# Kernel optimization log

Measured on AMD Instinct MI355X. Metric: run time of the kernel, lower is better.

## Reference

```python
import jax, jax.numpy as jnp
import numpy as np

N_LAYERS = 6
D_T = 6144   # d_transcoder (features per layer)
D_M = 768    # d_model (residual stream)
TOK = 128    # tokens (batch*seq)


def setup_inputs() -> dict:
    key = jax.random.key(0)
    k_x, k_enc, k_dec = jax.random.split(key, 3)
    x = jax.random.normal(k_x, (N_LAYERS, TOK, D_M), jnp.float32)
    W_enc = jax.random.normal(k_enc, (N_LAYERS, D_T, D_M), jnp.float32) * 0.02
    b_enc = jnp.zeros((N_LAYERS, D_T), jnp.float32)
    b_dec = jnp.zeros((N_LAYERS, D_M), jnp.float32)
    # Padded cross-layer decoder: W_dec[i, j] is the decoder from features at
    # layer i writing into layer j's MLP output; only j >= i is valid
    # (original stores a ragged list of [d_transcoder, n_layers - i, d_model]).
    W_dec = jax.random.normal(k_dec, (N_LAYERS, N_LAYERS, D_T, D_M), jnp.float32) * 0.02
    dec_mask = jnp.triu(jnp.ones((N_LAYERS, N_LAYERS), dtype=bool))  # mask[i, j] = (j >= i)
    W_dec = jnp.where(dec_mask[:, :, None, None], W_dec, 0.0)
    return {"x": x, "W_enc": W_enc, "b_enc": b_enc, "b_dec": b_dec,
            "W_dec": W_dec, "dec_mask": dec_mask}


def reference(x, W_enc, b_enc, b_dec, W_dec, dec_mask):
    # Encode: per-layer feature activations [n_layers, tok, d_transcoder]
    acts = jax.nn.relu(jnp.einsum('lnd,lfd->lnf', x, W_enc) + b_enc[:, None, :])
    # Decode: layer-i features write to all layers j >= i (mask enforces triangle)
    Wd = jnp.where(dec_mask[:, :, None, None], W_dec, 0.0)
    recon = jnp.einsum('inf,ijfd->jnd', acts, Wd) + b_dec[:, None, :]
    return recon  # [n_layers, tok, d_model]
```

## Files before the change

### kernel.cpp

```cpp
#include <hip/hip_runtime.h>
#include <hip/hip_bf16.h>

#define NL 6
#define DT 6144
#define DM 768
#define TOK 128

#define EF 32
#define EK 256
#define ENST (DM / EK)
#define NVE (2 * ENST)

#define TD 256
#define NTD 3
#define FC 768
#define NFC 8
#define NSTEP (FC / 32)
#define TILE_ELEMS (TOK * TD)

using bf16x8 = __attribute__((ext_vector_type(8))) short;
using f32x4  = __attribute__((ext_vector_type(4))) float;

typedef unsigned int u32;
typedef __attribute__((address_space(1))) const u32 gu32;
typedef __attribute__((address_space(3))) u32 lu32;

__device__ __forceinline__ void stage16(const float* g, float* l) {
  __builtin_amdgcn_global_load_lds((gu32*)g, (lu32*)l, 16, 0, 0);
}

#define ISSUE_FENCE() asm volatile("" ::: "memory")
#define VWAIT8() asm volatile("s_waitcnt vmcnt(8)" ::: "memory")
#define VWAIT0() asm volatile("s_waitcnt vmcnt(0)" ::: "memory")
#define RBAR()   asm volatile("s_barrier" ::: "memory")

__device__ __forceinline__ short f2bf(float f) {
  union { float f; unsigned u; } c; c.f = f;
  unsigned u = c.u;
  u += 0x7fffu + ((u >> 16) & 1u);
  return (short)(u >> 16);
}

__device__ __forceinline__ float bf2f(ushort u) {
  union { unsigned u; float f; } c; c.u = ((unsigned)u) << 16;
  return c.f;
}

__global__ void initcvt_k(const float* __restrict__ b_dec,
                          const float* __restrict__ x,
                          float* __restrict__ out, ushort* __restrict__ xb) {
  int idx = blockIdx.x * 256 + threadIdx.x;
  if (idx < NL * TOK * DM) {
    out[idx] = b_dec[(idx / (TOK * DM)) * DM + (idx % DM)];
    xb[idx] = (ushort)f2bf(x[idx]);
  }
}

__global__ __launch_bounds__(256, 2) void encode_k(
    const ushort* __restrict__ xb, const float* __restrict__ W_enc,
    const float* __restrict__ b_enc, ushort* __restrict__ acts)
{
  __shared__ float lw[2][EF][EK];

  const int l  = blockIdx.x / 96;
  const int fp = (blockIdx.x % 96) * 64;
  const int w    = threadIdx.x >> 6;
  const int lane = threadIdx.x & 63;
  const int lo = lane & 15, hi = lane >> 4;

  const float*  We = W_enc + ((size_t)l * DT + fp) * DM;
  const ushort* Xb = xb + (size_t)l * TOK * DM;

  f32x4 acc[2][2];
  #pragma unroll
  for (int mi = 0; mi < 2; ++mi)
    #pragma unroll
    for (int ni = 0; ni < 2; ++ni)
      acc[mi][ni] = f32x4{0.f, 0.f, 0.f, 0.f};

  #pragma unroll
  for (int q = 0; q < 8; ++q) {
    const int row = w * 8 + q;
    stage16(We + (size_t)row * DM + (lane ^ (row & 7)) * 4, &lw[0][row][0]);
  }
  __syncthreads();

  int cur = 0;
  #pragma unroll 1
  for (int v = 0; v < NVE; ++v) {
    const int tt = v / ENST;
    const int st = v % ENST;

    if (v + 1 < NVE) {
      const int tt2 = (v + 1) / ENST;
      const int st2 = (v + 1) % ENST;
      #pragma unroll
      for (int q = 0; q < 8; ++q) {
        const int row = w * 8 + q;
        stage16(We + (size_t)(tt2 * EF + row) * DM + st2 * EK + (lane ^ (row & 7)) * 4,
                &lw[cur ^ 1][row][0]);
      }
    }

    const int sw = lo & 7;
    #pragma unroll
    for (int ks = 0; ks < EK / 32; ++ks) {
      bf16x8 a[2], b[2];
      #pragma unroll
      for (int mi = 0; mi < 2; ++mi)
        a[mi] = *(const bf16x8*)(Xb + (size_t)(w * 32 + mi * 16 + lo) * DM
                                 + st * EK + ks * 32 + hi * 8);
      #pragma unroll
      for (int ni = 0; ni < 2; ++ni) {
        const int c0 = (ks * 8 + hi * 2) ^ sw;
        const int c1 = (ks * 8 + hi * 2 + 1) ^ sw;
        const float4 b0 = *(const float4*)&lw[cur][ni * 16 + lo][c0 * 4];
        const float4 b1 = *(const float4*)&lw[cur][ni * 16 + lo][c1 * 4];
        b[ni][0] = f2bf(b0.x); b[ni][1] = f2bf(b0.y);
        b[ni][2] = f2bf(b0.z); b[ni][3] = f2bf(b0.w);
        b[ni][4] = f2bf(b1.x); b[ni][5] = f2bf(b1.y);
        b[ni][6] = f2bf(b1.z); b[ni][7] = f2bf(b1.w);
      }

      #pragma unroll
      for (int mi = 0; mi < 2; ++mi)
        #pragma unroll
        for (int ni = 0; ni < 2; ++ni)
          acc[mi][ni] = __builtin_amdgcn_mfma_f32_16x16x32_bf16(a[mi], b[ni], acc[mi][ni], 0, 0, 0);
    }

    if (st == ENST - 1) {
      #pragma unroll
      for (int ni = 0; ni < 2; ++ni) {
        const int f = fp + tt * EF + ni * 16 + lo;
        const float bias = b_enc[l * DT + f];
        #pragma unroll
        for (int mi = 0; mi < 2; ++mi) {
          #pragma unroll
          for (int rr = 0; rr < 4; ++rr) {
            const int n = w * 32 + mi * 16 + hi * 4 + rr;
            float vv = acc[mi][ni][rr] + bias;
            vv = vv > 0.f ? vv : 0.f;
            acts[((size_t)l * TOK + n) * DT + f] = (ushort)f2bf(vv);
            acc[mi][ni][rr] = 0.f;
          }
        }
      }
    }

    __syncthreads();
    cur ^= 1;
  }
}

__device__ const int PI_[21]  = {0,0,0,0,0,0, 1,1,1,1,1, 2,2,2,2, 3,3,3, 4,4, 5};
__device__ const int PJ_[21]  = {0,1,2,3,4,5, 1,2,3,4,5, 2,3,4,5, 3,4,5, 4,5, 5};
__device__ const int OFFI_[6] = {0, 6, 11, 15, 18, 20};

__global__ __launch_bounds__(256, 2) void decode_part_k(
    const ushort* __restrict__ acts, const float* __restrict__ W_dec,
    ushort* __restrict__ part)
{
  __shared__ float lw[2][32][TD];

  const int xcd = blockIdx.x & 7;
  const int idx = blockIdx.x >> 3;
  const int logical = xcd * 63 + idx;
  const int p  = logical / (NFC * NTD);
  const int rm = logical % (NFC * NTD);
  const int c  = rm / NTD;
  const int t  = rm % NTD;
  const int i = PI_[p], j = PJ_[p];
  const int w = threadIdx.x >> 6;
  const int lane = threadIdx.x & 63;
  const int lo = lane & 15, hi = lane >> 4;
  const int fb = c * FC;
  (void)j;

  const float*  Wb = W_dec + ((size_t)(i * NL + j) * DT + fb) * DM + t * TD;
  const ushort* Ab = acts + (size_t)i * TOK * DT + fb;

  f32x4 acc[8][4];
  #pragma unroll
  for (int mi = 0; mi < 8; ++mi)
    #pragma unroll
    for (int ni = 0; ni < 4; ++ni)
      acc[mi][ni] = f32x4{0.f, 0.f, 0.f, 0.f};

  #pragma unroll
  for (int q = 0; q < 8; ++q) {
    const int row = w * 8 + q;
    stage16(Wb + (size_t)row * DM + lane * 4, &lw[0][row][0]);
  }

  int cur = 0;
  #pragma unroll 1
  for (int s = 0; s < NSTEP; ++s) {
    bf16x8 a[8];
    #pragma unroll
    for (int mi = 0; mi < 8; ++mi)
      a[mi] = *(const bf16x8*)(Ab + (size_t)(mi * 16 + lo) * DT + s * 32 + hi * 8);
    ISSUE_FENCE();

    if (s + 1 < NSTEP) {
      const float* Ws = Wb + (size_t)(s + 1) * 32 * DM;
      #pragma unroll
      for (int q = 0; q < 8; ++q) {
        const int row = w * 8 + q;
        stage16(Ws + (size_t)row * DM + lane * 4, &lw[cur ^ 1][row][0]);
      }
      VWAIT8();
    } else {
      VWAIT0();
    }
    RBAR();

    bf16x8 bb[4];
    #pragma unroll
    for (int ni = 0; ni < 4; ++ni) {
      const int col = w * 64 + ni * 16 + lo;
      #pragma unroll
      for (int e = 0; e < 8; ++e)
        bb[ni][e] = f2bf(lw[cur][hi * 8 + e][col]);
    }

    #pragma unroll
    for (int mi = 0; mi < 8; ++mi)
      #pragma unroll
      for (int ni = 0; ni < 4; ++ni)
        acc[mi][ni] = __builtin_amdgcn_mfma_f32_16x16x32_bf16(a[mi], bb[ni], acc[mi][ni], 0, 0, 0);

    RBAR();
    cur ^= 1;
  }

  ushort* pp = part + (size_t)logical * TILE_ELEMS;
  #pragma unroll
  for (int ni = 0; ni < 4; ++ni) {
    const int dl = w * 64 + ni * 16 + lo;
    #pragma unroll
    for (int mi = 0; mi < 8; ++mi)
      #pragma unroll
      for (int rr = 0; rr < 4; ++rr)
        pp[(size_t)(mi * 16 + hi * 4 + rr) * TD + dl] = (ushort)f2bf(acc[mi][ni][rr]);
  }
}

__global__ void reduce_k(const ushort* __restrict__ part,
                         const float* __restrict__ b_dec,
                         float* __restrict__ out)
{
  const int idx = blockIdx.x * 256 + threadIdx.x;
  if (idx >= NL * TOK * DM) return;
  const int j   = idx / (TOK * DM);
  const int rem = idx % (TOK * DM);
  const int n   = rem / DM;
  const int d   = rem % DM;
  const int t   = d >> 8;
  const int dl  = d & (TD - 1);

  float s = b_dec[j * DM + d];
  for (int i = 0; i <= j; ++i) {
    const int p = OFFI_[i] + (j - i);
    const ushort* pb = part + ((size_t)(p * NFC) * NTD + t) * TILE_ELEMS
                       + (size_t)n * TD + dl;
    #pragma unroll
    for (int c = 0; c < NFC; ++c)
      s += bf2f(pb[(size_t)c * NTD * TILE_ELEMS]);
  }
  out[idx] = s;
}

__global__ __launch_bounds__(256, 2) void decode_atomic_k(
    const ushort* __restrict__ acts, const float* __restrict__ W_dec,
    float* __restrict__ out)
{
  __shared__ float lw[2][32][TD];

  const int bid = blockIdx.x;
  const int p  = bid / (NTD * NFC);
  const int rm = bid % (NTD * NFC);
  const int c  = rm / NTD;
  const int t  = rm % NTD;
  const int i = PI_[p], j = PJ_[p];
  const int w = threadIdx.x >> 6;
  const int lane = threadIdx.x & 63;
  const int lo = lane & 15, hi = lane >> 4;
  const int fb = c * FC;

  const float*  Wb = W_dec + ((size_t)(i * NL + j) * DT + fb) * DM + t * TD;
  const ushort* Ab = acts + (size_t)i * TOK * DT + fb;

  f32x4 acc[8][4];
  #pragma unroll
  for (int mi = 0; mi < 8; ++mi)
    #pragma unroll
    for (int ni = 0; ni < 4; ++ni)
      acc[mi][ni] = f32x4{0.f, 0.f, 0.f, 0.f};

  #pragma unroll
  for (int q = 0; q < 8; ++q) {
    const int row = w * 8 + q;
    stage16(Wb + (size_t)row * DM + lane * 4, &lw[0][row][0]);
  }
  __syncthreads();

  int cur = 0;
  #pragma unroll 1
  for (int s = 0; s < NSTEP; ++s) {
    if (s + 1 < NSTEP) {
      const float* Ws = Wb + (size_t)(s + 1) * 32 * DM;
      #pragma unroll
      for (int q = 0; q < 8; ++q) {
        const int row = w * 8 + q;
        stage16(Ws + (size_t)row * DM + lane * 4, &lw[cur ^ 1][row][0]);
      }
    }

    bf16x8 a[8];
    #pragma unroll
    for (int mi = 0; mi < 8; ++mi)
      a[mi] = *(const bf16x8*)(Ab + (size_t)(mi * 16 + lo) * DT + s * 32 + hi * 8);

    bf16x8 bb[4];
    #pragma unroll
    for (int ni = 0; ni < 4; ++ni) {
      const int col = w * 64 + ni * 16 + lo;
      #pragma unroll
      for (int e = 0; e < 8; ++e)
        bb[ni][e] = f2bf(lw[cur][hi * 8 + e][col]);
    }

    #pragma unroll
    for (int mi = 0; mi < 8; ++mi)
      #pragma unroll
      for (int ni = 0; ni < 4; ++ni)
        acc[mi][ni] = __builtin_amdgcn_mfma_f32_16x16x32_bf16(a[mi], bb[ni], acc[mi][ni], 0, 0, 0);

    __syncthreads();
    cur ^= 1;
  }

  float* oj = out + (size_t)j * TOK * DM;
  #pragma unroll
  for (int ni = 0; ni < 4; ++ni) {
    const int d = t * TD + w * 64 + ni * 16 + lo;
    #pragma unroll
    for (int mi = 0; mi < 8; ++mi)
      #pragma unroll
      for (int rr = 0; rr < 4; ++rr)
        atomicAdd(oj + (size_t)(mi * 16 + hi * 4 + rr) * DM + d, acc[mi][ni][rr]);
  }
}

extern "C" void kernel_launch(void* const* d_in, const int* in_sizes, int n_in,
                              void* d_out, int out_size, void* d_ws, size_t ws_size,
                              hipStream_t stream) {
  const float* x     = (const float*)d_in[0];
  const float* W_enc = (const float*)d_in[1];
  const float* b_enc = (const float*)d_in[2];
  const float* b_dec = (const float*)d_in[3];
  const float* W_dec = (const float*)d_in[4];
  float* out = (float*)d_out;

  const size_t actsB = (size_t)NL * TOK * DT * 2;
  const size_t xbB   = (size_t)NL * TOK * DM * 2;
  const size_t partB = (size_t)21 * NFC * NTD * TILE_ELEMS * 2;

  ushort* acts = (ushort*)d_ws;
  ushort* xb   = (ushort*)((char*)d_ws + actsB);
  ushort* part = (ushort*)((char*)d_ws + actsB + xbB);

  initcvt_k<<<dim3((NL * TOK * DM + 255) / 256), dim3(256), 0, stream>>>(b_dec, x, out, xb);
  encode_k<<<dim3(NL * 96), dim3(256), 0, stream>>>(xb, W_enc, b_enc, acts);

  if (ws_size >= actsB + xbB + partB) {
    decode_part_k<<<dim3(21 * NFC * NTD), dim3(256), 0, stream>>>(acts, W_dec, part);
    reduce_k<<<dim3((NL * TOK * DM + 255) / 256), dim3(256), 0, stream>>>(part, b_dec, out);
  } else {
    decode_atomic_k<<<dim3(21 * NFC * NTD), dim3(256), 0, stream>>>(acts, W_dec, out);
  }
}
```

Before: 184.2 us.

## Stage decoder weights through registers with two-step-ahead prefetch, drop XCD remap

The decode kernel no longer uses global_load_lds direct-to-LDS staging. Each thread now loads W_dec tiles into two register sets two K-steps ahead and writes them into the double-buffered LDS after computing, which leaves one barrier per step instead of two. The block-to-tile mapping also drops the XCD-interleaved remap and uses blockIdx directly. The aim is deeper prefetch and less barrier stalling. The cost is 64 extra VGPRs per thread and possibly worse L2 locality across XCDs.

```diff
diff --git a/kernel.cpp b/kernel.cpp
--- a/kernel.cpp
+++ b/kernel.cpp
@@ -32,6 +32,7 @@
 #define ISSUE_FENCE() asm volatile("" ::: "memory")
 #define VWAIT8() asm volatile("s_waitcnt vmcnt(8)" ::: "memory")
 #define VWAIT0() asm volatile("s_waitcnt vmcnt(0)" ::: "memory")
+#define LGKM0()  asm volatile("s_waitcnt lgkmcnt(0)" ::: "memory")
 #define RBAR()   asm volatile("s_barrier" ::: "memory")
 
 __device__ __forceinline__ short f2bf(float f) {
@@ -157,17 +158,55 @@
 __device__ const int PJ_[21]  = {0,1,2,3,4,5, 1,2,3,4,5, 2,3,4,5, 3,4,5, 4,5, 5};
 __device__ const int OFFI_[6] = {0, 6, 11, 15, 18, 20};
 
+#define LOADR(R, S)                                                          \
+  {                                                                          \
+    const float* Ws_ = Wb + (size_t)(S) * 32 * DM;                           \
+    _Pragma("unroll")                                                        \
+    for (int q = 0; q < 8; ++q)                                              \
+      R[q] = *(const float4*)(Ws_ + (size_t)(w * 8 + q) * DM + lane * 4);    \
+  }
+
+#define WRITEB(R, BUF)                                                       \
+  {                                                                          \
+    _Pragma("unroll")                                                        \
+    for (int q = 0; q < 8; ++q)                                              \
+      *(float4*)&lw[BUF][w * 8 + q][lane * 4] = R[q];                        \
+  }
+
+#define ALOAD(S)                                                             \
+  bf16x8 a[8];                                                               \
+  _Pragma("unroll")                                                          \
+  for (int mi = 0; mi < 8; ++mi)                                             \
+    a[mi] = *(const bf16x8*)(Ab + (size_t)(mi * 16 + lo) * DT + (S) * 32 + hi * 8);
+
+#define COMPUTE(BUF)                                                         \
+  {                                                                          \
+    bf16x8 bb[4];                                                            \
+    _Pragma("unroll")                                                        \
+    for (int ni = 0; ni < 4; ++ni) {                                         \
+      const int col = w * 64 + ni * 16 + lo;                                 \
+      _Pragma("unroll")                                                      \
+      for (int e = 0; e < 8; ++e)                                            \
+        bb[ni][e] = f2bf(lw[BUF][hi * 8 + e][col]);                          \
+    }                                                                        \
+    _Pragma("unroll")                                                        \
+    for (int mi = 0; mi < 8; ++mi) {                                         \
+      _Pragma("unroll")                                                      \
+      for (int ni = 0; ni < 4; ++ni)                                         \
+        acc[mi][ni] = __builtin_amdgcn_mfma_f32_16x16x32_bf16(               \
+            a[mi], bb[ni], acc[mi][ni], 0, 0, 0);                            \
+    }                                                                        \
+  }
+
 __global__ __launch_bounds__(256, 2) void decode_part_k(
     const ushort* __restrict__ acts, const float* __restrict__ W_dec,
     ushort* __restrict__ part)
 {
   __shared__ float lw[2][32][TD];
 
-  const int xcd = blockIdx.x & 7;
-  const int idx = blockIdx.x >> 3;
-  const int logical = xcd * 63 + idx;
-  const int p  = logical / (NFC * NTD);
-  const int rm = logical % (NFC * NTD);
+  const int bid = blockIdx.x;
+  const int p  = bid / (NFC * NTD);
+  const int rm = bid % (NFC * NTD);
   const int c  = rm / NTD;
   const int t  = rm % NTD;
   const int i = PI_[p], j = PJ_[p];
@@ -187,54 +226,40 @@
     for (int ni = 0; ni < 4; ++ni)
       acc[mi][ni] = f32x4{0.f, 0.f, 0.f, 0.f};
 
-  #pragma unroll
-  for (int q = 0; q < 8; ++q) {
-    const int row = w * 8 + q;
-    stage16(Wb + (size_t)row * DM + lane * 4, &lw[0][row][0]);
-  }
-
-  int cur = 0;
+  float4 rA[8], rB[8];
+
+  LOADR(rA, 0);
+  ISSUE_FENCE();
+  LOADR(rB, 1);
+  WRITEB(rA, 0);
+  LGKM0();
+  RBAR();
+
   #pragma unroll 1
-  for (int s = 0; s < NSTEP; ++s) {
-    bf16x8 a[8];
-    #pragma unroll
-    for (int mi = 0; mi < 8; ++mi)
-      a[mi] = *(const bf16x8*)(Ab + (size_t)(mi * 16 + lo) * DT + s * 32 + hi * 8);
-    ISSUE_FENCE();
-
-    if (s + 1 < NSTEP) {
-      const float* Ws = Wb + (size_t)(s + 1) * 32 * DM;
-      #pragma unroll
-      for (int q = 0; q < 8; ++q) {
-        const int row = w * 8 + q;
-        stage16(Ws + (size_t)row * DM + lane * 4, &lw[cur ^ 1][row][0]);
+  for (int s = 0; s < NSTEP; s += 2) {
+    {
+      ALOAD(s);
+      ISSUE_FENCE();
+      if (s + 2 < NSTEP) { LOADR(rA, s + 2); VWAIT8(); } else { VWAIT0(); }
+      COMPUTE(0);
+      WRITEB(rB, 1);
+      LGKM0();
+      RBAR();
+    }
+    {
+      ALOAD(s + 1);
+      ISSUE_FENCE();
+      if (s + 3 < NSTEP) { LOADR(rB, s + 3); VWAIT8(); } else { VWAIT0(); }
+      COMPUTE(1);
+      if (s + 2 < NSTEP) {
+        WRITEB(rA, 0);
+        LGKM0();
+        RBAR();
       }
-      VWAIT8();
-    } else {
-      VWAIT0();
-    }
-    RBAR();
-
-    bf16x8 bb[4];
-    #pragma unroll
-    for (int ni = 0; ni < 4; ++ni) {
-      const int col = w * 64 + ni * 16 + lo;
-      #pragma unroll
-      for (int e = 0; e < 8; ++e)
-        bb[ni][e] = f2bf(lw[cur][hi * 8 + e][col]);
-    }
-
-    #pragma unroll
-    for (int mi = 0; mi < 8; ++mi)
-      #pragma unroll
-      for (int ni = 0; ni < 4; ++ni)
-        acc[mi][ni] = __builtin_amdgcn_mfma_f32_16x16x32_bf16(a[mi], bb[ni], acc[mi][ni], 0, 0, 0);
-
-    RBAR();
-    cur ^= 1;
-  }
-
-  ushort* pp = part + (size_t)logical * TILE_ELEMS;
+    }
+  }
+
+  ushort* pp = part + (size_t)bid * TILE_ELEMS;
   #pragma unroll
   for (int ni = 0; ni < 4; ++ni) {
     const int dl = w * 64 + ni * 16 + lo;
```

Result: slower. 285.9 us (+55.3%).
